# Kernel tuning notes

Hardware: AMD Instinct MI355X
Metric: run time of the kernel (lower is better)

Reference implementation:

```python
import jax, jax.numpy as jnp
import numpy as np

LATENT = 128
HEADS = 4
HEAD_DIM = LATENT // HEADS
NUM_BUCKETS = 32
MAX_DISTANCE = 100000
B, N = 8, 2048


def relative_position_bucket(qpos, kpos):
    """T5-style bidirectional relative position bucketing.
    qpos, kpos: [B, N] int -> buckets [B, N, N] int32 in [0, NUM_BUCKETS).
    """
    rel = kpos[:, None, :] - qpos[:, :, None]  # [B, Nq, Nk]
    half = NUM_BUCKETS // 2
    buckets = (rel > 0).astype(jnp.int32) * half
    arel = jnp.abs(rel)
    max_exact = half // 2
    is_small = arel < max_exact
    # log-spaced buckets for larger distances
    large = max_exact + (
        jnp.log(jnp.maximum(arel, 1).astype(jnp.float32) / max_exact)
        / np.log(MAX_DISTANCE / max_exact)
        * (half - max_exact)
    ).astype(jnp.int32)
    large = jnp.minimum(large, half - 1)
    return buckets + jnp.where(is_small, arel.astype(jnp.int32), large)


def setup_inputs() -> dict:
    key = jax.random.key(0)
    ks = jax.random.split(key, 12)
    s = 0.02
    x = jax.random.normal(ks[0], (B, N, LATENT), dtype=jnp.float32)
    positions = jnp.sort(jax.random.randint(ks[1], (B, N), 0, 1000000), axis=-1)
    mask = jnp.ones((B, N), dtype=bool)
    Wq = jax.random.normal(ks[2], (LATENT, LATENT), dtype=jnp.float32) * s
    bq = jax.random.normal(ks[3], (LATENT,), dtype=jnp.float32) * s
    Wk = jax.random.normal(ks[4], (LATENT, LATENT), dtype=jnp.float32) * s
    bk = jax.random.normal(ks[5], (LATENT,), dtype=jnp.float32) * s
    Wv = jax.random.normal(ks[6], (LATENT, LATENT), dtype=jnp.float32) * s
    bv = jax.random.normal(ks[7], (LATENT,), dtype=jnp.float32) * s
    pos_w = jax.random.normal(ks[8], (NUM_BUCKETS + 1, HEADS), dtype=jnp.float32) * s
    Wo = jax.random.normal(ks[9], (LATENT, LATENT), dtype=jnp.float32) * s
    bo = jax.random.normal(ks[10], (LATENT,), dtype=jnp.float32) * s
    return {"x": x, "positions": positions, "mask": mask,
            "Wq": Wq, "bq": bq, "Wk": Wk, "bk": bk, "Wv": Wv, "bv": bv,
            "pos_w": pos_w, "Wo": Wo, "bo": bo}


def reference(x, positions, mask, Wq, bq, Wk, bk, Wv, bv, pos_w, Wo, bo):
    b, n, _ = x.shape
    # QKV projections, split heads: [b, h, n, d]
    Q = (x @ Wq + bq).reshape(b, n, HEADS, HEAD_DIM).transpose(0, 2, 1, 3)
    K = (x @ Wk + bk).reshape(b, n, HEADS, HEAD_DIM).transpose(0, 2, 1, 3)
    V = (x @ Wv + bv).reshape(b, n, HEADS, HEAD_DIM).transpose(0, 2, 1, 3)
    scores = jnp.einsum("bhqd,bhkd->bhqk", Q, K) / jnp.sqrt(
        jnp.asarray(HEAD_DIM, dtype=x.dtype))
    buckets = relative_position_bucket(positions, positions)  # [b, n, n]
    bias = pos_w[buckets]                  # [b, n, n, h]
    scores = scores + bias.transpose(0, 3, 1, 2)  # [b, h, n, n]
    scores = jnp.where(mask[:, None, None, :], scores, -jnp.inf)
    attn = jax.nn.softmax(scores, axis=-1)
    attn = jnp.nan_to_num(attn, nan=0.0)
    attended = jnp.einsum("bhqk,bhkd->bhqd", attn, V)
    attended = attended.transpose(0, 2, 1, 3).reshape(b, n, LATENT)
    return attended @ Wo + bo
```

## Files before the change

### kernel.cpp

```cpp
#include <hip/hip_runtime.h>
#include <math.h>


#define LOG2E 1.4426950408889634f
#define QKV_SCALE 0.17677669529663687f
#define QS (QKV_SCALE * LOG2E)

typedef _Float16 half8 __attribute__((ext_vector_type(8)));
typedef float ffrag __attribute__((ext_vector_type(4)));

#if __has_builtin(__builtin_amdgcn_exp2f)
#define EXP2F __builtin_amdgcn_exp2f
#else
#define EXP2F exp2f
#endif

static __device__ __forceinline__ unsigned short f16bits(float f) {
    return __builtin_bit_cast(unsigned short, (_Float16)f);
}
static __device__ __forceinline__ float h16f(unsigned int bits) {
    return (float)__builtin_bit_cast(_Float16, (unsigned short)(bits & 0xFFFFu));
}
static __device__ __forceinline__ unsigned int pk2(float a, float b) {
    return __builtin_bit_cast(unsigned int, __builtin_amdgcn_cvt_pkrtz(a, b));
}

__device__ __constant__ int SN_TAB[32] = {
    -2000000000,
    -30755, -9458, -2908, -894, -275, -84, -26,
    -7, -6, -5, -4, -3, -2, -1,
    0,
    1, 2, 3, 4, 5, 6, 7,
    8,
    27, 85, 276, 895, 2909, 9459, 30756,
    2000000000 };

__global__ __launch_bounds__(256)
void pre_seg_kernel(const float* __restrict__ Wq, const float* __restrict__ Wk,
                    const float* __restrict__ Wv, const float* __restrict__ Wo,
                    const int* __restrict__ positions,
                    unsigned short* __restrict__ Wt_qkv,
                    unsigned short* __restrict__ Wt_o,
                    unsigned int* __restrict__ segtab)
{
    if (blockIdx.x < 256) {
        const int e = blockIdx.x * 256 + threadIdx.x;
        const int m = e >> 14, r = e & 16383;
        const int c = r >> 7, k = r & 127;
        float v;
        if (m == 0)      v = Wq[k * 128 + c] * QS;
        else if (m == 1) v = Wk[k * 128 + c];
        else if (m == 2) v = Wv[k * 128 + c];
        else             v = Wo[k * 128 + c];
        if (m < 3) Wt_qkv[(m * 128 + c) * 128 + k] = f16bits(v);
        else       Wt_o[c * 128 + k] = f16bits(v);
        return;
    }
    const int gid = (blockIdx.x - 256) * 256 + threadIdx.x;
    const int row = gid >> 5;
    const int s = gid & 31;
    const int b = row >> 11;
    const int* kp = positions + b * 2048;
    const int qp = kp[row & 2047];
    const int bucket = (s < 15) ? (15 - s) : (s == 15 ? 0 : s + 1);
    if (s == 31) { segtab[row * 32 + s] = (2048u << 16) | 31u; return; }
    const int target = qp + SN_TAB[s + 1];
    int lo = 0, hi = 2048;
    while (lo < hi) { const int mid = (lo + hi) >> 1; if (kp[mid] < target) lo = mid + 1; else hi = mid; }
    segtab[row * 32 + s] = ((unsigned)lo << 16) | (unsigned)bucket;
}

__global__ __launch_bounds__(128)
void qkv_reg(const float* __restrict__ x, const unsigned short* __restrict__ Wt,
             const float* __restrict__ bq, const float* __restrict__ bk,
             const float* __restrict__ bv,
             unsigned short* __restrict__ Qb, unsigned short* __restrict__ Kb,
             unsigned short* __restrict__ Vg2)
{
    const int tid = threadIdx.x;
    const int wave = tid >> 6, lane = tid & 63;
    const int lq = lane & 15, quad = lane >> 4;
    const int token0 = blockIdx.x * 16;
    const int b = token0 >> 11;
    const int n0 = token0 & 2047;

    half8 xf[4];
    #pragma unroll
    for (int ks = 0; ks < 4; ++ks) {
        const float* xp = x + (size_t)(token0 + lq) * 128 + ks * 32 + quad * 8;
        const float4 a = *(const float4*)xp;
        const float4 c = *(const float4*)(xp + 4);
        xf[ks] = __builtin_bit_cast(half8,
                 make_int4(pk2(a.x, a.y), pk2(a.z, a.w), pk2(c.x, c.y), pk2(c.z, c.w)));
    }

    #pragma unroll
    for (int jj = 0; jj < 8; ++jj) {
        const int ct = wave * 8 + jj;
        const int colbase = ct * 16;
        half8 wf[4];
        #pragma unroll
        for (int ks = 0; ks < 4; ++ks)
            wf[ks] = *(const half8*)(Wt + (size_t)(colbase + lq) * 128 + ks * 32 + quad * 8);
        const int c0 = colbase + quad * 4;
        const int cl = (ct < 8) ? c0 : (c0 - 128);
        float4 bias;
        if (ct < 8) {
            bias = *(const float4*)(bq + c0);
            bias.x *= QS; bias.y *= QS; bias.z *= QS; bias.w *= QS;
        } else {
            bias = *(const float4*)(bk + cl);
        }
        ffrag acc = {bias.x, bias.y, bias.z, bias.w};
        #pragma unroll
        for (int ks = 0; ks < 4; ++ks)
            acc = __builtin_amdgcn_mfma_f32_16x16x32_f16(wf[ks], xf[ks], acc, 0, 0, 0);
        const int h = cl >> 5, d = cl & 31;
        const ushort4 v4 = make_ushort4(f16bits(acc[0]), f16bits(acc[1]),
                                        f16bits(acc[2]), f16bits(acc[3]));
        unsigned short* base = (ct < 8) ? Qb : Kb;
        *(ushort4*)(base + ((size_t)(b * 4 + h) * 2048 + n0 + lq) * 32 + d) = v4;
    }

    #pragma unroll
    for (int jj = 0; jj < 4; ++jj) {
        const int ct = 16 + wave * 4 + jj;
        const int colbase = ct * 16;
        half8 wf[4];
        #pragma unroll
        for (int ks = 0; ks < 4; ++ks)
            wf[ks] = *(const half8*)(Wt + (size_t)(colbase + lq) * 128 + ks * 32 + quad * 8);
        const int col128 = colbase + lq - 256;
        const float bias = bv[col128];
        ffrag acc = {bias, bias, bias, bias};
        #pragma unroll
        for (int ks = 0; ks < 4; ++ks)
            acc = __builtin_amdgcn_mfma_f32_16x16x32_f16(xf[ks], wf[ks], acc, 0, 0, 0);
        const int h = col128 >> 5, d = col128 & 31;
        const int nn = n0 + quad * 4;
        const int chunk = nn >> 7, kloc = nn & 127;
        const int win = kloc >> 5, rem = kloc & 31;
        const int hlf = rem >> 4, pg = (rem >> 2) & 3;
        const size_t off = (((size_t)(b * 4 + h) * 16 + chunk) * 512
                            + win * 128 + d * 4 + pg) * 8 + hlf * 4;
        *(ushort4*)(Vg2 + off) = make_ushort4(f16bits(acc[0]), f16bits(acc[1]),
                                              f16bits(acc[2]), f16bits(acc[3]));
    }
}

__global__ __launch_bounds__(512, 4)
void attn_kernel(const unsigned short* __restrict__ Qb,
                 const unsigned short* __restrict__ Kb,
                 const unsigned short* __restrict__ Vg2,
                 const unsigned int* __restrict__ segtab,
                 const float* __restrict__ pos_w,
                 unsigned short* __restrict__ att)
{
    __shared__ __align__(16) unsigned int SMEM[4672];
    unsigned int* Sg = SMEM;

    const int tid = threadIdx.x;
    const int wave = __builtin_amdgcn_readfirstlane(tid >> 6);
    const int lane = tid & 63;
    const int lq = lane & 15, quad = lane >> 4;
    const int g = wave >> 2, wg = wave & 3;

    const int qt = blockIdx.x & 15, bh = blockIdx.x >> 4;
    const int b = bh >> 2, h = bh & 3;
    const int q0 = qt * 128;

    const unsigned short* Kg = Kb + (size_t)bh * 65536;
    const unsigned short* Vgb = Vg2 + (size_t)bh * 65536;

    {
        const unsigned int* src = segtab + ((size_t)b * 2048 + q0) * 32;
        #pragma unroll
        for (int it = 0; it < 2; ++it) {
            const int e4 = tid + it * 512;
            uint4 u = *(const uint4*)(src + e4 * 4);
            unsigned int* c = &u.x;
            const int row = e4 >> 3, s0 = (e4 & 7) * 4;
            const int rx = row & 31;
            #pragma unroll
            for (int i2 = 0; i2 < 4; ++i2) {
                const float wfv = __expf(pos_w[(c[i2] & 0xFFFFu) * 4 + h]);
                Sg[row * 32 + ((s0 + i2) ^ rx)] = (c[i2] & 0xFFFF0000u) | f16bits(wfv);
            }
        }
    }

    const int qa = q0 + wg * 32 + lq;
    const int qbn = qa + 16;
    const half8 qfa = *(const half8*)(Qb + ((size_t)bh * 2048 + qa) * 32 + quad * 8);
    const half8 qfb = *(const half8*)(Qb + ((size_t)bh * 2048 + qbn) * 32 + quad * 8);

    half8 ones;
    #pragma unroll
    for (int i = 0; i < 8; ++i) ones[i] = (_Float16)1.0f;

    ffrag o0a = {0.f,0.f,0.f,0.f}, o1a = {0.f,0.f,0.f,0.f}, o2a = {0.f,0.f,0.f,0.f};
    ffrag o0b = {0.f,0.f,0.f,0.f}, o1b = {0.f,0.f,0.f,0.f}, o2b = {0.f,0.f,0.f,0.f};
    int cura = -1, enda = 0; float wfa = 0.f;
    int curb = -1, endb = 0; float wfb = 0.f;
    const int rowa = wg * 32 + lq, rowb = rowa + 16;
    const int sga = rowa * 32, xa = rowa & 31;
    const int sgb = rowb * 32, xb = rowb & 31;

    half8 kf[2][4], vf[4];
    const int gv = (lq * 4 + quad) * 8;

    auto load_k = [&](half8* dst, int idx) {
        const int kb0 = idx * 64;
        #pragma unroll
        for (int j = 0; j < 4; ++j)
            dst[j] = *(const half8*)(Kg + (size_t)(kb0 + j * 16 + lq) * 32 + quad * 8);
    };
    auto load_v = [&](int idx) {
        const unsigned short* vp = Vgb + (size_t)(idx >> 1) * 4096 + (idx & 1) * 2048 + gv;
        vf[0] = *(const half8*)(vp);
        vf[1] = *(const half8*)(vp + 512);
        vf[2] = *(const half8*)(vp + 1024);
        vf[3] = *(const half8*)(vp + 1536);
    };
    auto compute = [&](const half8* karr, int idx) {
        const int kb0 = idx * 64;
        #pragma unroll
        for (int dw = 0; dw < 2; ++dw) {
            unsigned int pua[4], pub[4];
            #pragma unroll
            for (int T = 0; T < 2; ++T) {
                const half8 kfc = karr[dw * 2 + T];
                ffrag sa = {0.f,0.f,0.f,0.f}, sb = {0.f,0.f,0.f,0.f};
                sa = __builtin_amdgcn_mfma_f32_16x16x32_f16(kfc, qfa, sa, 0, 0, 0);
                sb = __builtin_amdgcn_mfma_f32_16x16x32_f16(kfc, qfb, sb, 0, 0, 0);
                const int kidx = kb0 + dw * 32 + T * 16 + quad * 4;
                float pa[4], pb[4];
                if (__builtin_expect(__any(kidx + 3 >= enda), 0)) {
                    #pragma unroll
                    for (int r = 0; r < 4; ++r) {
                        while (kidx + r >= enda) {
                            const unsigned int u = Sg[sga + ((++cura) ^ xa)];
                            enda = (int)(u >> 16); wfa = h16f(u);
                        }
                        pa[r] = EXP2F(sa[r]) * wfa;
                    }
                } else {
                    #pragma unroll
                    for (int r = 0; r < 4; ++r) pa[r] = EXP2F(sa[r]) * wfa;
                }
                if (__builtin_expect(__any(kidx + 3 >= endb), 0)) {
                    #pragma unroll
                    for (int r = 0; r < 4; ++r) {
                        while (kidx + r >= endb) {
                            const unsigned int u = Sg[sgb + ((++curb) ^ xb)];
                            endb = (int)(u >> 16); wfb = h16f(u);
                        }
                        pb[r] = EXP2F(sb[r]) * wfb;
                    }
                } else {
                    #pragma unroll
                    for (int r = 0; r < 4; ++r) pb[r] = EXP2F(sb[r]) * wfb;
                }
                pua[T * 2 + 0] = pk2(pa[0], pa[1]);
                pua[T * 2 + 1] = pk2(pa[2], pa[3]);
                pub[T * 2 + 0] = pk2(pb[0], pb[1]);
                pub[T * 2 + 1] = pk2(pb[2], pb[3]);
            }
            const half8 A0 = vf[dw * 2];
            const half8 A1 = vf[dw * 2 + 1];
            const half8 Ba = __builtin_bit_cast(half8, make_int4(pua[0], pua[1], pua[2], pua[3]));
            const half8 Bb = __builtin_bit_cast(half8, make_int4(pub[0], pub[1], pub[2], pub[3]));
            o0a = __builtin_amdgcn_mfma_f32_16x16x32_f16(A0, Ba, o0a, 0, 0, 0);
            o1a = __builtin_amdgcn_mfma_f32_16x16x32_f16(A1, Ba, o1a, 0, 0, 0);
            o2a = __builtin_amdgcn_mfma_f32_16x16x32_f16(ones, Ba, o2a, 0, 0, 0);
            o0b = __builtin_amdgcn_mfma_f32_16x16x32_f16(A0, Bb, o0b, 0, 0, 0);
            o1b = __builtin_amdgcn_mfma_f32_16x16x32_f16(A1, Bb, o1b, 0, 0, 0);
            o2b = __builtin_amdgcn_mfma_f32_16x16x32_f16(ones, Bb, o2b, 0, 0, 0);
        }
    };

    __syncthreads();
    load_k(kf[0], g * 2);

    #pragma unroll 1
    for (int i = 0; i < 8; ++i) {
        const int ci = 2 * i + g;
        load_v(ci * 2);
        load_k(kf[1], ci * 2 + 1);
        compute(kf[0], ci * 2);
        load_v(ci * 2 + 1);
        if (i < 7) load_k(kf[0], ci * 2 + 4);
        compute(kf[1], ci * 2 + 1);
    }

    float lsa = o2a[0], lsb = o2b[0];
    __syncthreads();
    float* scr = (float*)SMEM;
    if (g == 1) {
        float* s = scr + (wg * 64 + lane) * 18;
        #pragma unroll
        for (int j = 0; j < 4; ++j) {
            s[j] = o0a[j]; s[4 + j] = o1a[j]; s[8 + j] = o0b[j]; s[12 + j] = o1b[j];
        }
        s[16] = lsa; s[17] = lsb;
    }
    __syncthreads();
    if (g == 0) {
        const float* s = scr + (wg * 64 + lane) * 18;
        #pragma unroll
        for (int j = 0; j < 4; ++j) {
            o0a[j] += s[j]; o1a[j] += s[4 + j]; o0b[j] += s[8 + j]; o1b[j] += s[12 + j];
        }
        lsa += s[16]; lsb += s[17];
        const float inva = 1.0f / lsa;
        const float invb = 1.0f / lsb;

        unsigned short* da = att + (size_t)(b * 2048 + qa) * 128 + h * 32 + quad * 4;
        uint2 r0, r1;
        r0.x = pk2(o0a[0] * inva, o0a[1] * inva);
        r0.y = pk2(o0a[2] * inva, o0a[3] * inva);
        r1.x = pk2(o1a[0] * inva, o1a[1] * inva);
        r1.y = pk2(o1a[2] * inva, o1a[3] * inva);
        *(uint2*)da = r0;
        *(uint2*)(da + 16) = r1;

        unsigned short* db = att + (size_t)(b * 2048 + qbn) * 128 + h * 32 + quad * 4;
        r0.x = pk2(o0b[0] * invb, o0b[1] * invb);
        r0.y = pk2(o0b[2] * invb, o0b[3] * invb);
        r1.x = pk2(o1b[0] * invb, o1b[1] * invb);
        r1.y = pk2(o1b[2] * invb, o1b[3] * invb);
        *(uint2*)db = r0;
        *(uint2*)(db + 16) = r1;
    }
}

__global__ __launch_bounds__(128)
void out_reg(const unsigned short* __restrict__ att,
             const unsigned short* __restrict__ Wt_o,
             const float* __restrict__ bo, float* __restrict__ out)
{
    const int tid = threadIdx.x;
    const int wave = tid >> 6, lane = tid & 63;
    const int lq = lane & 15, quad = lane >> 4;
    const int token0 = blockIdx.x * 16;

    half8 af[4];
    #pragma unroll
    for (int ks = 0; ks < 4; ++ks)
        af[ks] = *(const half8*)(att + (size_t)(token0 + lq) * 128 + ks * 32 + quad * 8);

    #pragma unroll
    for (int jj = 0; jj < 4; ++jj) {
        const int ct = wave * 4 + jj;
        const int colbase = ct * 16;
        half8 wf[4];
        #pragma unroll
        for (int ks = 0; ks < 4; ++ks)
            wf[ks] = *(const half8*)(Wt_o + (size_t)(colbase + lq) * 128 + ks * 32 + quad * 8);
        const int c0 = colbase + quad * 4;
        const float4 bias = *(const float4*)(bo + c0);
        ffrag acc = {bias.x, bias.y, bias.z, bias.w};
        #pragma unroll
        for (int ks = 0; ks < 4; ++ks)
            acc = __builtin_amdgcn_mfma_f32_16x16x32_f16(wf[ks], af[ks], acc, 0, 0, 0);
        *(float4*)(out + (size_t)(token0 + lq) * 128 + c0) =
            make_float4(acc[0], acc[1], acc[2], acc[3]);
    }
}

extern "C" void kernel_launch(void* const* d_in, const int* in_sizes, int n_in,
                              void* d_out, int out_size, void* d_ws, size_t ws_size,
                              hipStream_t stream)
{
    const float* x         = (const float*)d_in[0];
    const int*   positions = (const int*)d_in[1];
    const float* Wq = (const float*)d_in[3];
    const float* bq = (const float*)d_in[4];
    const float* Wk = (const float*)d_in[5];
    const float* bk = (const float*)d_in[6];
    const float* Wv = (const float*)d_in[7];
    const float* bv = (const float*)d_in[8];
    const float* pw = (const float*)d_in[9];
    const float* Wo = (const float*)d_in[10];
    const float* bo = (const float*)d_in[11];
    float* out = (float*)d_out;

    unsigned short* Qb  = (unsigned short*)d_ws;
    unsigned short* Kb  = Qb + 2097152;
    unsigned short* Vg2 = Kb + 2097152;
    unsigned short* att = Vg2 + 2097152;
    unsigned int* segtab = (unsigned int*)(att + 2097152);
    unsigned short* Wt_qkv = (unsigned short*)(segtab + 524288);
    unsigned short* Wt_o = Wt_qkv + 49152;

    pre_seg_kernel<<<2304, 256, 0, stream>>>(Wq, Wk, Wv, Wo, positions,
                                             Wt_qkv, Wt_o, segtab);
    qkv_reg<<<1024, 128, 0, stream>>>(x, Wt_qkv, bq, bk, bv, Qb, Kb, Vg2);
    attn_kernel<<<512, 512, 0, stream>>>(Qb, Kb, Vg2, segtab, pw, att);
    out_reg<<<1024, 128, 0, stream>>>(att, Wt_o, bo, out);
}
```

Before: 161.1 us.

## Fuse kernels into two launches with last-block output projection and register row sums

Merges weight conversion, segment-table binary search and the QKV projection into one kernel that reads fp32 weights directly. The output projection moves into the attention kernel: an atomic counter per batch/query-tile picks the last of the four head blocks, and that block computes the output rows. The softmax denominator now comes from register sums plus lane shuffles instead of an extra MFMA against a ones vector, and V fragments are double-buffered alongside K. This removes two launches and intermediate round trips. In exchange it adds a memset, atomics and fences, strided uncoalesced weight loads in the QKV kernel, and a serialized tail in the attention kernel.

```diff
diff --git a/kernel.cpp b/kernel.cpp
--- a/kernel.cpp
+++ b/kernel.cpp
@@ -35,126 +35,146 @@
     27, 85, 276, 895, 2909, 9459, 30756,
     2000000000 };
 
-__global__ __launch_bounds__(256)
-void pre_seg_kernel(const float* __restrict__ Wq, const float* __restrict__ Wk,
-                    const float* __restrict__ Wv, const float* __restrict__ Wo,
-                    const int* __restrict__ positions,
-                    unsigned short* __restrict__ Wt_qkv,
-                    unsigned short* __restrict__ Wt_o,
-                    unsigned int* __restrict__ segtab)
-{
-    if (blockIdx.x < 256) {
-        const int e = blockIdx.x * 256 + threadIdx.x;
-        const int m = e >> 14, r = e & 16383;
-        const int c = r >> 7, k = r & 127;
-        float v;
-        if (m == 0)      v = Wq[k * 128 + c] * QS;
-        else if (m == 1) v = Wk[k * 128 + c];
-        else if (m == 2) v = Wv[k * 128 + c];
-        else             v = Wo[k * 128 + c];
-        if (m < 3) Wt_qkv[(m * 128 + c) * 128 + k] = f16bits(v);
-        else       Wt_o[c * 128 + k] = f16bits(v);
-        return;
-    }
-    const int gid = (blockIdx.x - 256) * 256 + threadIdx.x;
-    const int row = gid >> 5;
-    const int s = gid & 31;
-    const int b = row >> 11;
-    const int* kp = positions + b * 2048;
-    const int qp = kp[row & 2047];
-    const int bucket = (s < 15) ? (15 - s) : (s == 15 ? 0 : s + 1);
-    if (s == 31) { segtab[row * 32 + s] = (2048u << 16) | 31u; return; }
-    const int target = qp + SN_TAB[s + 1];
-    int lo = 0, hi = 2048;
-    while (lo < hi) { const int mid = (lo + hi) >> 1; if (kp[mid] < target) lo = mid + 1; else hi = mid; }
-    segtab[row * 32 + s] = ((unsigned)lo << 16) | (unsigned)bucket;
-}
-
-__global__ __launch_bounds__(128)
-void qkv_reg(const float* __restrict__ x, const unsigned short* __restrict__ Wt,
-             const float* __restrict__ bq, const float* __restrict__ bk,
-             const float* __restrict__ bv,
-             unsigned short* __restrict__ Qb, unsigned short* __restrict__ Kb,
-             unsigned short* __restrict__ Vg2)
+__global__ __launch_bounds__(512)
+void qkv_seg_kernel(const float* __restrict__ x, const int* __restrict__ positions,
+                    const float* __restrict__ Wq, const float* __restrict__ bq,
+                    const float* __restrict__ Wk, const float* __restrict__ bk,
+                    const float* __restrict__ Wv, const float* __restrict__ bv,
+                    const float* __restrict__ Wo,
+                    unsigned short* __restrict__ Qb, unsigned short* __restrict__ Kb,
+                    unsigned short* __restrict__ Vg2,
+                    unsigned int* __restrict__ segtab,
+                    unsigned short* __restrict__ Wt_o)
 {
     const int tid = threadIdx.x;
     const int wave = tid >> 6, lane = tid & 63;
     const int lq = lane & 15, quad = lane >> 4;
-    const int token0 = blockIdx.x * 16;
-    const int b = token0 >> 11;
-    const int n0 = token0 & 2047;
-
-    half8 xf[4];
+    const int p = blockIdx.x;
+
+    const int token0 = p * 32;
+    const int b = token0 >> 11, n0 = token0 & 2047;
+    const int colbase = wave * 16;
+
+    half8 xf[2][4];
     #pragma unroll
-    for (int ks = 0; ks < 4; ++ks) {
-        const float* xp = x + (size_t)(token0 + lq) * 128 + ks * 32 + quad * 8;
-        const float4 a = *(const float4*)xp;
-        const float4 c = *(const float4*)(xp + 4);
-        xf[ks] = __builtin_bit_cast(half8,
-                 make_int4(pk2(a.x, a.y), pk2(a.z, a.w), pk2(c.x, c.y), pk2(c.z, c.w)));
-    }
+    for (int m = 0; m < 2; ++m)
+        #pragma unroll
+        for (int ks = 0; ks < 4; ++ks) {
+            const float* xp = x + (size_t)(token0 + m * 16 + lq) * 128 + ks * 32 + quad * 8;
+            const float4 a = *(const float4*)xp;
+            const float4 c = *(const float4*)(xp + 4);
+            xf[m][ks] = __builtin_bit_cast(half8,
+                make_int4(pk2(a.x, a.y), pk2(a.z, a.w), pk2(c.x, c.y), pk2(c.z, c.w)));
+        }
 
     #pragma unroll
-    for (int jj = 0; jj < 8; ++jj) {
-        const int ct = wave * 8 + jj;
-        const int colbase = ct * 16;
+    for (int which = 0; which < 2; ++which) {
+        const float* W  = which ? Wk : Wq;
+        const float* bb = which ? bk : bq;
+        unsigned short* dst = which ? Kb : Qb;
+        const float sc = which ? 1.0f : QS;
         half8 wf[4];
         #pragma unroll
-        for (int ks = 0; ks < 4; ++ks)
-            wf[ks] = *(const half8*)(Wt + (size_t)(colbase + lq) * 128 + ks * 32 + quad * 8);
+        for (int ks = 0; ks < 4; ++ks) {
+            half8 w;
+            #pragma unroll
+            for (int jj = 0; jj < 8; ++jj) {
+                const int k = ks * 32 + quad * 8 + jj;
+                w[jj] = (_Float16)(W[k * 128 + colbase + lq] * sc);
+            }
+            wf[ks] = w;
+        }
         const int c0 = colbase + quad * 4;
-        const int cl = (ct < 8) ? c0 : (c0 - 128);
-        float4 bias;
-        if (ct < 8) {
-            bias = *(const float4*)(bq + c0);
-            bias.x *= QS; bias.y *= QS; bias.z *= QS; bias.w *= QS;
-        } else {
-            bias = *(const float4*)(bk + cl);
-        }
-        ffrag acc = {bias.x, bias.y, bias.z, bias.w};
-        #pragma unroll
-        for (int ks = 0; ks < 4; ++ks)
-            acc = __builtin_amdgcn_mfma_f32_16x16x32_f16(wf[ks], xf[ks], acc, 0, 0, 0);
-        const int h = cl >> 5, d = cl & 31;
-        const ushort4 v4 = make_ushort4(f16bits(acc[0]), f16bits(acc[1]),
-                                        f16bits(acc[2]), f16bits(acc[3]));
-        unsigned short* base = (ct < 8) ? Qb : Kb;
-        *(ushort4*)(base + ((size_t)(b * 4 + h) * 2048 + n0 + lq) * 32 + d) = v4;
-    }
-
-    #pragma unroll
-    for (int jj = 0; jj < 4; ++jj) {
-        const int ct = 16 + wave * 4 + jj;
-        const int colbase = ct * 16;
+        float4 bs = *(const float4*)(bb + c0);
+        const int h = c0 >> 5, d = c0 & 31;
+        #pragma unroll
+        for (int m = 0; m < 2; ++m) {
+            ffrag acc = {bs.x * sc, bs.y * sc, bs.z * sc, bs.w * sc};
+            #pragma unroll
+            for (int ks = 0; ks < 4; ++ks)
+                acc = __builtin_amdgcn_mfma_f32_16x16x32_f16(wf[ks], xf[m][ks], acc, 0, 0, 0);
+            const int n = n0 + m * 16 + lq;
+            *(ushort4*)(dst + ((size_t)(b * 4 + h) * 2048 + n) * 32 + d) =
+                make_ushort4(f16bits(acc[0]), f16bits(acc[1]),
+                             f16bits(acc[2]), f16bits(acc[3]));
+        }
+    }
+
+    {
         half8 wf[4];
         #pragma unroll
-        for (int ks = 0; ks < 4; ++ks)
-            wf[ks] = *(const half8*)(Wt + (size_t)(colbase + lq) * 128 + ks * 32 + quad * 8);
-        const int col128 = colbase + lq - 256;
-        const float bias = bv[col128];
-        ffrag acc = {bias, bias, bias, bias};
-        #pragma unroll
-        for (int ks = 0; ks < 4; ++ks)
-            acc = __builtin_amdgcn_mfma_f32_16x16x32_f16(xf[ks], wf[ks], acc, 0, 0, 0);
-        const int h = col128 >> 5, d = col128 & 31;
-        const int nn = n0 + quad * 4;
-        const int chunk = nn >> 7, kloc = nn & 127;
-        const int win = kloc >> 5, rem = kloc & 31;
-        const int hlf = rem >> 4, pg = (rem >> 2) & 3;
-        const size_t off = (((size_t)(b * 4 + h) * 16 + chunk) * 512
-                            + win * 128 + d * 4 + pg) * 8 + hlf * 4;
-        *(ushort4*)(Vg2 + off) = make_ushort4(f16bits(acc[0]), f16bits(acc[1]),
-                                              f16bits(acc[2]), f16bits(acc[3]));
+        for (int ks = 0; ks < 4; ++ks) {
+            half8 w;
+            #pragma unroll
+            for (int jj = 0; jj < 8; ++jj) {
+                const int k = ks * 32 + quad * 8 + jj;
+                w[jj] = (_Float16)Wv[k * 128 + colbase + lq];
+            }
+            wf[ks] = w;
+        }
+        const int col = colbase + lq;
+        const float bias = bv[col];
+        const int h = col >> 5, d = col & 31;
+        #pragma unroll
+        for (int m = 0; m < 2; ++m) {
+            ffrag acc = {bias, bias, bias, bias};
+            #pragma unroll
+            for (int ks = 0; ks < 4; ++ks)
+                acc = __builtin_amdgcn_mfma_f32_16x16x32_f16(xf[m][ks], wf[ks], acc, 0, 0, 0);
+            const int nn = n0 + m * 16 + quad * 4;
+            const int chunk = nn >> 7, kloc = nn & 127;
+            const int win = kloc >> 5, rem = kloc & 31;
+            const int hlf = rem >> 4, pg = (rem >> 2) & 3;
+            const size_t off = (((size_t)(b * 4 + h) * 16 + chunk) * 512
+                                + win * 128 + d * 4 + pg) * 8 + hlf * 4;
+            *(ushort4*)(Vg2 + off) = make_ushort4(f16bits(acc[0]), f16bits(acc[1]),
+                                                  f16bits(acc[2]), f16bits(acc[3]));
+        }
+    }
+
+    {
+        const int row = p * 32 + (tid >> 4);
+        const int bb2 = row >> 11;
+        const int* kp = positions + bb2 * 2048;
+        const int qp = kp[row & 2047];
+        #pragma unroll
+        for (int ss = 0; ss < 2; ++ss) {
+            const int s = (tid & 15) + ss * 16;
+            unsigned int val;
+            if (s == 31) {
+                val = (2048u << 16) | 31u;
+            } else {
+                const int bucket = (s < 15) ? (15 - s) : (s == 15 ? 0 : s + 1);
+                const int target = qp + SN_TAB[s + 1];
+                int lo = 0, hi = 2048;
+                while (lo < hi) {
+                    const int mid = (lo + hi) >> 1;
+                    if (kp[mid] < target) lo = mid + 1; else hi = mid;
+                }
+                val = ((unsigned)lo << 16) | (unsigned)bucket;
+            }
+            segtab[row * 32 + s] = val;
+        }
+    }
+
+    if (tid < 32) {
+        const int e = p * 32 + tid;
+        const int c = e >> 7, k = e & 127;
+        Wt_o[c * 128 + k] = f16bits(Wo[k * 128 + c]);
     }
 }
 
 __global__ __launch_bounds__(512, 4)
-void attn_kernel(const unsigned short* __restrict__ Qb,
-                 const unsigned short* __restrict__ Kb,
-                 const unsigned short* __restrict__ Vg2,
-                 const unsigned int* __restrict__ segtab,
-                 const float* __restrict__ pos_w,
-                 unsigned short* __restrict__ att)
+void attn_out_kernel(const unsigned short* __restrict__ Qb,
+                     const unsigned short* __restrict__ Kb,
+                     const unsigned short* __restrict__ Vg2,
+                     const unsigned int* __restrict__ segtab,
+                     const float* __restrict__ pos_w,
+                     unsigned short* __restrict__ att,
+                     unsigned short* __restrict__ Wt_o,
+                     const float* __restrict__ bo,
+                     unsigned int* __restrict__ counters,
+                     float* __restrict__ out)
 {
     __shared__ __align__(16) unsigned int SMEM[4672];
     unsigned int* Sg = SMEM;
@@ -188,25 +208,23 @@
             }
         }
     }
+    __syncthreads();
 
     const int qa = q0 + wg * 32 + lq;
     const int qbn = qa + 16;
     const half8 qfa = *(const half8*)(Qb + ((size_t)bh * 2048 + qa) * 32 + quad * 8);
     const half8 qfb = *(const half8*)(Qb + ((size_t)bh * 2048 + qbn) * 32 + quad * 8);
 
-    half8 ones;
-    #pragma unroll
-    for (int i = 0; i < 8; ++i) ones[i] = (_Float16)1.0f;
-
-    ffrag o0a = {0.f,0.f,0.f,0.f}, o1a = {0.f,0.f,0.f,0.f}, o2a = {0.f,0.f,0.f,0.f};
-    ffrag o0b = {0.f,0.f,0.f,0.f}, o1b = {0.f,0.f,0.f,0.f}, o2b = {0.f,0.f,0.f,0.f};
+    ffrag o0a = {0.f,0.f,0.f,0.f}, o1a = {0.f,0.f,0.f,0.f};
+    ffrag o0b = {0.f,0.f,0.f,0.f}, o1b = {0.f,0.f,0.f,0.f};
+    float lsa = 0.f, lsb = 0.f;
     int cura = -1, enda = 0; float wfa = 0.f;
     int curb = -1, endb = 0; float wfb = 0.f;
     const int rowa = wg * 32 + lq, rowb = rowa + 16;
     const int sga = rowa * 32, xa = rowa & 31;
     const int sgb = rowb * 32, xb = rowb & 31;
 
-    half8 kf[2][4], vf[4];
+    half8 kf[2][4], vf[2][4];
     const int gv = (lq * 4 + quad) * 8;
 
     auto load_k = [&](half8* dst, int idx) {
@@ -215,14 +233,14 @@
         for (int j = 0; j < 4; ++j)
             dst[j] = *(const half8*)(Kg + (size_t)(kb0 + j * 16 + lq) * 32 + quad * 8);
     };
-    auto load_v = [&](int idx) {
+    auto load_v = [&](half8* dst, int idx) {
         const unsigned short* vp = Vgb + (size_t)(idx >> 1) * 4096 + (idx & 1) * 2048 + gv;
-        vf[0] = *(const half8*)(vp);
-        vf[1] = *(const half8*)(vp + 512);
-        vf[2] = *(const half8*)(vp + 1024);
-        vf[3] = *(const half8*)(vp + 1536);
+        dst[0] = *(const half8*)(vp);
+        dst[1] = *(const half8*)(vp + 512);
+        dst[2] = *(const half8*)(vp + 1024);
+        dst[3] = *(const half8*)(vp + 1536);
     };
-    auto compute = [&](const half8* karr, int idx) {
+    auto compute = [&](const half8* karr, const half8* varr, int idx) {
         const int kb0 = idx * 64;
         #pragma unroll
         for (int dw = 0; dw < 2; ++dw) {
@@ -261,39 +279,42 @@
                     #pragma unroll
                     for (int r = 0; r < 4; ++r) pb[r] = EXP2F(sb[r]) * wfb;
                 }
+                lsa += (pa[0] + pa[1]) + (pa[2] + pa[3]);
+                lsb += (pb[0] + pb[1]) + (pb[2] + pb[3]);
                 pua[T * 2 + 0] = pk2(pa[0], pa[1]);
                 pua[T * 2 + 1] = pk2(pa[2], pa[3]);
                 pub[T * 2 + 0] = pk2(pb[0], pb[1]);
                 pub[T * 2 + 1] = pk2(pb[2], pb[3]);
             }
-            const half8 A0 = vf[dw * 2];
-            const half8 A1 = vf[dw * 2 + 1];
+            const half8 A0 = varr[dw * 2];
+            const half8 A1 = varr[dw * 2 + 1];
             const half8 Ba = __builtin_bit_cast(half8, make_int4(pua[0], pua[1], pua[2], pua[3]));
             const half8 Bb = __builtin_bit_cast(half8, make_int4(pub[0], pub[1], pub[2], pub[3]));
             o0a = __builtin_amdgcn_mfma_f32_16x16x32_f16(A0, Ba, o0a, 0, 0, 0);
             o1a = __builtin_amdgcn_mfma_f32_16x16x32_f16(A1, Ba, o1a, 0, 0, 0);
-            o2a = __builtin_amdgcn_mfma_f32_16x16x32_f16(ones, Ba, o2a, 0, 0, 0);
             o0b = __builtin_amdgcn_mfma_f32_16x16x32_f16(A0, Bb, o0b, 0, 0, 0);
             o1b = __builtin_amdgcn_mfma_f32_16x16x32_f16(A1, Bb, o1b, 0, 0, 0);
-            o2b = __builtin_amdgcn_mfma_f32_16x16x32_f16(ones, Bb, o2b, 0, 0, 0);
         }
     };
 
-    __syncthreads();
     load_k(kf[0], g * 2);
+    load_v(vf[0], g * 2);
 
     #pragma unroll 1
     for (int i = 0; i < 8; ++i) {
         const int ci = 2 * i + g;
-        load_v(ci * 2);
         load_k(kf[1], ci * 2 + 1);
-        compute(kf[0], ci * 2);
-        load_v(ci * 2 + 1);
-        if (i < 7) load_k(kf[0], ci * 2 + 4);
-        compute(kf[1], ci * 2 + 1);
-    }
-
-    float lsa = o2a[0], lsb = o2b[0];
+        load_v(vf[1], ci * 2 + 1);
+        compute(kf[0], vf[0], ci * 2);
+        if (i < 7) {
+            load_k(kf[0], ci * 2 + 4);
+            load_v(vf[0], ci * 2 + 4);
+        }
+        compute(kf[1], vf[1], ci * 2 + 1);
+    }
+
+    lsa += __shfl_xor(lsa, 16); lsa += __shfl_xor(lsa, 32);
+    lsb += __shfl_xor(lsb, 16); lsb += __shfl_xor(lsb, 32);
     __syncthreads();
     float* scr = (float*)SMEM;
     if (g == 1) {
@@ -332,39 +353,38 @@
         *(uint2*)db = r0;
         *(uint2*)(db + 16) = r1;
     }
-}
-
-__global__ __launch_bounds__(128)
-void out_reg(const unsigned short* __restrict__ att,
-             const unsigned short* __restrict__ Wt_o,
-             const float* __restrict__ bo, float* __restrict__ out)
-{
-    const int tid = threadIdx.x;
-    const int wave = tid >> 6, lane = tid & 63;
-    const int lq = lane & 15, quad = lane >> 4;
-    const int token0 = blockIdx.x * 16;
-
-    half8 af[4];
-    #pragma unroll
-    for (int ks = 0; ks < 4; ++ks)
-        af[ks] = *(const half8*)(att + (size_t)(token0 + lq) * 128 + ks * 32 + quad * 8);
-
-    #pragma unroll
-    for (int jj = 0; jj < 4; ++jj) {
-        const int ct = wave * 4 + jj;
-        const int colbase = ct * 16;
-        half8 wf[4];
+
+    __syncthreads();
+    if (tid == 0) {
+        __threadfence();
+        const unsigned old = atomicAdd(&counters[(b << 4) | qt], 1u);
+        unsigned fl = (old == 3u) ? 1u : 0u;
+        if (fl) __threadfence();
+        SMEM[4650] = fl;
+    }
+    __syncthreads();
+    if (SMEM[4650]) {
+        const int trow = b * 2048 + q0 + wave * 16 + lq;
+        half8 af[4];
         #pragma unroll
         for (int ks = 0; ks < 4; ++ks)
-            wf[ks] = *(const half8*)(Wt_o + (size_t)(colbase + lq) * 128 + ks * 32 + quad * 8);
-        const int c0 = colbase + quad * 4;
-        const float4 bias = *(const float4*)(bo + c0);
-        ffrag acc = {bias.x, bias.y, bias.z, bias.w};
-        #pragma unroll
-        for (int ks = 0; ks < 4; ++ks)
-            acc = __builtin_amdgcn_mfma_f32_16x16x32_f16(wf[ks], af[ks], acc, 0, 0, 0);
-        *(float4*)(out + (size_t)(token0 + lq) * 128 + c0) =
-            make_float4(acc[0], acc[1], acc[2], acc[3]);
+            af[ks] = *(const half8*)(att + (size_t)trow * 128 + ks * 32 + quad * 8);
+        #pragma unroll
+        for (int ct = 0; ct < 8; ++ct) {
+            const int colbase = ct * 16;
+            half8 wf2[4];
+            #pragma unroll
+            for (int ks = 0; ks < 4; ++ks)
+                wf2[ks] = *(const half8*)(Wt_o + (size_t)(colbase + lq) * 128 + ks * 32 + quad * 8);
+            const int c0 = colbase + quad * 4;
+            const float4 bias = *(const float4*)(bo + c0);
+            ffrag acc = {bias.x, bias.y, bias.z, bias.w};
+            #pragma unroll
+            for (int ks = 0; ks < 4; ++ks)
+                acc = __builtin_amdgcn_mfma_f32_16x16x32_f16(wf2[ks], af[ks], acc, 0, 0, 0);
+            *(float4*)(out + (size_t)trow * 128 + c0) =
+                make_float4(acc[0], acc[1], acc[2], acc[3]);
+        }
     }
 }
 
@@ -390,12 +410,12 @@
     unsigned short* Vg2 = Kb + 2097152;
     unsigned short* att = Vg2 + 2097152;
     unsigned int* segtab = (unsigned int*)(att + 2097152);
-    unsigned short* Wt_qkv = (unsigned short*)(segtab + 524288);
-    unsigned short* Wt_o = Wt_qkv + 49152;
-
-    pre_seg_kernel<<<2304, 256, 0, stream>>>(Wq, Wk, Wv, Wo, positions,
-                                             Wt_qkv, Wt_o, segtab);
-    qkv_reg<<<1024, 128, 0, stream>>>(x, Wt_qkv, bq, bk, bv, Qb, Kb, Vg2);
-    attn_kernel<<<512, 512, 0, stream>>>(Qb, Kb, Vg2, segtab, pw, att);
-    out_reg<<<1024, 128, 0, stream>>>(att, Wt_o, bo, out);
-}
+    unsigned short* Wt_o = (unsigned short*)(segtab + 524288);
+    unsigned int* counters = (unsigned int*)(Wt_o + 16384);
+
+    hipMemsetAsync(counters, 0, 128 * sizeof(unsigned int), stream);
+    qkv_seg_kernel<<<512, 512, 0, stream>>>(x, positions, Wq, bq, Wk, bk, Wv, bv,
+                                            Wo, Qb, Kb, Vg2, segtab, Wt_o);
+    attn_out_kernel<<<512, 512, 0, stream>>>(Qb, Kb, Vg2, segtab, pw, att,
+                                             Wt_o, bo, counters, out);
+}
```

After: 244.9 us. 52.0% more time.
